# Performance work log

Hardware: AMD Instinct MI355X
Metric: run time of the kernel (lower is better)

Reference implementation:

```python
import jax, jax.numpy as jnp
import numpy as np

N, K, E, H, I = 4096, 2, 8, 2048, 1408  # tokens, top_k, experts, hidden, intermediate


def setup_inputs() -> dict:
    key = jax.random.key(0)
    kx, kl, kg, ku, kd = jax.random.split(key, 5)
    x = jax.random.normal(kx, (N, H), dtype=jnp.float32)
    # routing: distinct top-k expert ids per token (matches scatter_-based counting)
    logits = jax.random.normal(kl, (N, E), dtype=jnp.float32)
    top_vals, topk_ids = jax.lax.top_k(logits, K)
    topk_weight = jax.nn.softmax(top_vals, axis=-1)
    sH = 1.0 / np.sqrt(H).astype(np.float32)
    sI = 1.0 / np.sqrt(I).astype(np.float32)
    Wg = jax.random.normal(kg, (E, I, H), dtype=jnp.float32) * sH  # gate_proj per expert
    Wu = jax.random.normal(ku, (E, I, H), dtype=jnp.float32) * sH  # up_proj per expert
    Wd = jax.random.normal(kd, (E, H, I), dtype=jnp.float32) * sI  # down_proj per expert
    return {"x": x, "topk_ids": topk_ids.astype(jnp.int32), "topk_weight": topk_weight,
            "Wg": Wg, "Wu": Wu, "Wd": Wd}


def reference(x, topk_ids, topk_weight, Wg, Wu, Wd):
    # SwiGLU MLP for every expert on every token (dense reference for the
    # sort/dispatch/combine loop), then gather the top_k expert outputs and
    # combine with routing weights -- identical math to the torch module.
    g = jnp.einsum('nh,eih->eni', x, Wg)           # [E, N, I]
    u = jnp.einsum('nh,eih->eni', x, Wu)           # [E, N, I]
    hidden = jax.nn.silu(g) * u                    # fused SwiGLU
    out = jnp.einsum('eni,ehi->neh', hidden, Wd)   # [N, E, H]
    sel = jnp.take_along_axis(out, topk_ids[..., None].astype(jnp.int32), axis=1)  # [N, K, H]
    return jnp.sum(sel * topk_weight[..., None], axis=1)  # [N, H]
```

## Files before the change

### kernel.cpp

```cpp
#include <hip/hip_runtime.h>
#include <stdint.h>

#define N_TOK 4096
#define TOPK  2
#define NEXP  8
#define HID   2048
#define INTER 1408
#define NSLOT (N_TOK * TOPK)
#define PADROWS 128
#define WELEM (NEXP * INTER * HID)
#define MAXTILES 72

typedef _Float16 half8 __attribute__((ext_vector_type(8)));
typedef float floatx4 __attribute__((ext_vector_type(4)));

__device__ __forceinline__ void gld_lds16(const void* g, void* l) {
  __builtin_amdgcn_global_load_lds(
      (const __attribute__((address_space(1))) uint32_t*)g,
      (__attribute__((address_space(3))) uint32_t*)l, 16, 0, 0);
}

#define WAITCNT_VM6   0x0F76
#define WAITCNT_VM4   0x0F74
#define WAITCNT_VM0   0x0F70
#define WAITCNT_LGKM0 0xC07F
#define RAW_BARRIER() asm volatile("s_barrier" ::: "memory")

__global__ void route_kernel(const int* __restrict__ ids, const float* __restrict__ tw,
                             int* __restrict__ tinfo,
                             int* __restrict__ stok, float* __restrict__ sw) {
  __shared__ int tc[NEXP][257];
  __shared__ int eo[NEXP + 1];
  const int t = threadIdx.x;
  int lc[NEXP];
#pragma unroll
  for (int e = 0; e < NEXP; e++) lc[e] = 0;
  for (int i = 0; i < NSLOT / 256; i++) {
    int e = ids[t + 256 * i];
#pragma unroll
    for (int q = 0; q < NEXP; q++) lc[q] += (e == q) ? 1 : 0;
  }
#pragma unroll
  for (int e = 0; e < NEXP; e++) tc[e][t + 1] = lc[e];
  if (t < NEXP) tc[t][0] = 0;
  __syncthreads();
  if (t < NEXP) {
    int run = 0;
    for (int i = 0; i <= 256; i++) { run += tc[t][i]; tc[t][i] = run; }
  }
  __syncthreads();
  if (t == 0) {
    eo[0] = 0;
    for (int e = 0; e < NEXP; e++) eo[e + 1] = eo[e] + tc[e][256];
    int nt = 0;
    for (int e = 0; e < NEXP; e++) {
      const int c = tc[e][256];
      for (int r0 = 0; r0 < c; r0 += 128) {
        tinfo[1 + 3 * nt] = e;
        tinfo[2 + 3 * nt] = eo[e] + r0;
        tinfo[3 + 3 * nt] = (c - r0 < 128) ? (c - r0) : 128;
        nt++;
      }
    }
    tinfo[0] = nt;
  }
  __syncthreads();
  int pos[NEXP];
#pragma unroll
  for (int e = 0; e < NEXP; e++) pos[e] = eo[e] + tc[e][t];
  for (int i = 0; i < NSLOT / 256; i++) {
    int s = t + 256 * i;
    int e = ids[s];
    int p = 0;
#pragma unroll
    for (int q = 0; q < NEXP; q++)
      if (e == q) p = pos[q]++;
    stok[p] = s / TOPK;
    sw[p] = tw[s];
  }
}

__global__ void gather_x_kernel(const float* __restrict__ x, const int* __restrict__ stok,
                                _Float16* __restrict__ xg) {
  const int row = blockIdx.x;
  const int tok = stok[row];
  const float4* src = (const float4*)(x + (size_t)tok * HID);
  half8* dst = (half8*)(xg + (size_t)row * HID);
  const int t = threadIdx.x;
  float4 a = src[2 * t], b = src[2 * t + 1];
  half8 h;
  h[0] = (_Float16)a.x; h[1] = (_Float16)a.y; h[2] = (_Float16)a.z; h[3] = (_Float16)a.w;
  h[4] = (_Float16)b.x; h[5] = (_Float16)b.y; h[6] = (_Float16)b.z; h[7] = (_Float16)b.w;
  dst[t] = h;
}

__global__ void convert3_kernel(const float* __restrict__ s0, const float* __restrict__ s1,
                                const float* __restrict__ s2, _Float16* __restrict__ d0,
                                _Float16* __restrict__ d1, _Float16* __restrict__ d2) {
  const float* s = blockIdx.z == 0 ? s0 : (blockIdx.z == 1 ? s1 : s2);
  _Float16* d = blockIdx.z == 0 ? d0 : (blockIdx.z == 1 ? d1 : d2);
  const int j = (blockIdx.x * 256 + threadIdx.x) * 8;
  float4 a = *(const float4*)(s + j);
  float4 b = *(const float4*)(s + j + 4);
  half8 h;
  h[0] = (_Float16)a.x; h[1] = (_Float16)a.y; h[2] = (_Float16)a.z; h[3] = (_Float16)a.w;
  h[4] = (_Float16)b.x; h[5] = (_Float16)b.y; h[6] = (_Float16)b.z; h[7] = (_Float16)b.w;
  *(half8*)(d + j) = h;
}

__global__ void zero_kernel(float4* __restrict__ p, int n4) {
  int i = blockIdx.x * blockDim.x + threadIdx.x;
  int stride = gridDim.x * blockDim.x;
  for (; i < n4; i += stride) p[i] = make_float4(0.f, 0.f, 0.f, 0.f);
}

__global__ __launch_bounds__(256, 2) void gateup_kernel(
    const _Float16* __restrict__ A, const _Float16* __restrict__ Bg,
    const _Float16* __restrict__ Bu, _Float16* __restrict__ H,
    const int* __restrict__ tinfo) {
  const int nt = tinfo[0];
  const int ty = blockIdx.y;
  if (ty >= nt) return;
  const int e    = tinfo[1 + 3 * ty];
  const int row0 = tinfo[2 + 3 * ty];
  const int mrem = tinfo[3 + 3 * ty];
  const int col0 = blockIdx.x * 128;
  const _Float16* Bge = Bg + (size_t)e * INTER * HID;
  const _Float16* Bue = Bu + (size_t)e * INTER * HID;

  __shared__ __align__(16) _Float16 As[2][128 * 32];
  __shared__ __align__(16) _Float16 Bgs[2][128 * 32];
  __shared__ __align__(16) _Float16 Bus[2][128 * 32];

  const int tid = threadIdx.x;
  const int wave = tid >> 6, lane = tid & 63;
  const int quad = lane >> 4, l16 = lane & 15;
  const int wm = (wave >> 1) * 64, wn = (wave & 1) * 64;

  const int bo0 = wave * 2048 + lane * 16, bo1 = bo0 + 1024;
  const int ar0 = bo0 >> 6, ak0 = (bo0 & 63) >> 1;
  const int ar1 = bo1 >> 6, ak1 = (bo1 & 63) >> 1;
  const _Float16* Ab0 = A + (size_t)(row0 + ar0) * HID + ak0;
  const _Float16* Ab1 = A + (size_t)(row0 + ar1) * HID + ak1;
  const _Float16* Bg0 = Bge + (size_t)(col0 + ar0) * HID + ak0;
  const _Float16* Bg1 = Bge + (size_t)(col0 + ar1) * HID + ak1;
  const _Float16* Bu0 = Bue + (size_t)(col0 + ar0) * HID + ak0;
  const _Float16* Bu1 = Bue + (size_t)(col0 + ar1) * HID + ak1;

  floatx4 ag[4][4], au[4][4];
#pragma unroll
  for (int a = 0; a < 4; a++)
#pragma unroll
    for (int b = 0; b < 4; b++) {
      ag[a][b] = (floatx4){0.f, 0.f, 0.f, 0.f};
      au[a][b] = (floatx4){0.f, 0.f, 0.f, 0.f};
    }

  auto stage = [&](int kt, int buf) {
    const int k0 = kt * 32;
    char* as = (char*)(As[buf]) + wave * 2048;
    char* bg = (char*)(Bgs[buf]) + wave * 2048;
    char* bu = (char*)(Bus[buf]) + wave * 2048;
    gld_lds16(Ab0 + k0, as);
    gld_lds16(Ab1 + k0, as + 1024);
    gld_lds16(Bg0 + k0, bg);
    gld_lds16(Bg1 + k0, bg + 1024);
    gld_lds16(Bu0 + k0, bu);
    gld_lds16(Bu1 + k0, bu + 1024);
  };

  const int NKI = HID / 32;
  stage(0, 0);
  stage(1, 1);
  for (int kt = 0; kt < NKI; ++kt) {
    const int buf = kt & 1;
    if (kt < NKI - 1) __builtin_amdgcn_s_waitcnt(WAITCNT_VM6);
    else              __builtin_amdgcn_s_waitcnt(WAITCNT_VM0);
    RAW_BARRIER();
    half8 af[4], bgf[4], buf_[4];
#pragma unroll
    for (int i = 0; i < 4; ++i) {
      af[i]   = *(const half8*)(As[buf]  + (wm + i * 16 + l16) * 32 + quad * 8);
      bgf[i]  = *(const half8*)(Bgs[buf] + (wn + i * 16 + l16) * 32 + quad * 8);
      buf_[i] = *(const half8*)(Bus[buf] + (wn + i * 16 + l16) * 32 + quad * 8);
    }
    __builtin_amdgcn_s_waitcnt(WAITCNT_LGKM0);
    RAW_BARRIER();
    if (kt + 2 < NKI) stage(kt + 2, buf);
#pragma unroll
    for (int mi = 0; mi < 4; ++mi)
#pragma unroll
      for (int ni = 0; ni < 4; ++ni) {
        ag[mi][ni] = __builtin_amdgcn_mfma_f32_16x16x32_f16(af[mi], bgf[ni], ag[mi][ni], 0, 0, 0);
        au[mi][ni] = __builtin_amdgcn_mfma_f32_16x16x32_f16(af[mi], buf_[ni], au[mi][ni], 0, 0, 0);
      }
  }

#pragma unroll
  for (int mi = 0; mi < 4; ++mi)
#pragma unroll
    for (int r = 0; r < 4; ++r) {
      const int rm = wm + mi * 16 + quad * 4 + r;
      if (rm < mrem) {
        _Float16* hrow = H + (size_t)(row0 + rm) * INTER + col0 + wn;
#pragma unroll
        for (int ni = 0; ni < 4; ++ni) {
          float g = ag[mi][ni][r], u = au[mi][ni][r];
          float s = 1.0f / (1.0f + __expf(-g));
          hrow[ni * 16 + l16] = (_Float16)(g * s * u);
        }
      }
    }
}

__global__ __launch_bounds__(256, 3) void down_kernel(
    const _Float16* __restrict__ A, const _Float16* __restrict__ B, float* __restrict__ out,
    const int* __restrict__ tinfo, const int* __restrict__ stok, const float* __restrict__ sw) {
  const int nt = tinfo[0];
  const int ty = blockIdx.y;
  if (ty >= nt) return;
  const int e    = tinfo[1 + 3 * ty];
  const int row0 = tinfo[2 + 3 * ty];
  const int mrem = tinfo[3 + 3 * ty];
  const int col0 = blockIdx.x * 128;
  const _Float16* Be = B + (size_t)e * HID * INTER;

  __shared__ __align__(16) _Float16 As[2][128 * 32];
  __shared__ __align__(16) _Float16 Bs[2][128 * 32];

  const int tid = threadIdx.x;
  const int wave = tid >> 6, lane = tid & 63;
  const int quad = lane >> 4, l16 = lane & 15;
  const int wm = (wave >> 1) * 64, wn = (wave & 1) * 64;

  const int bo0 = wave * 2048 + lane * 16, bo1 = bo0 + 1024;
  const int ar0 = bo0 >> 6, ak0 = (bo0 & 63) >> 1;
  const int ar1 = bo1 >> 6, ak1 = (bo1 & 63) >> 1;
  const _Float16* Ab0 = A + (size_t)(row0 + ar0) * INTER + ak0;
  const _Float16* Ab1 = A + (size_t)(row0 + ar1) * INTER + ak1;
  const _Float16* Bb0 = Be + (size_t)(col0 + ar0) * INTER + ak0;
  const _Float16* Bb1 = Be + (size_t)(col0 + ar1) * INTER + ak1;

  floatx4 acc[4][4];
#pragma unroll
  for (int a = 0; a < 4; a++)
#pragma unroll
    for (int b = 0; b < 4; b++) acc[a][b] = (floatx4){0.f, 0.f, 0.f, 0.f};

  auto stage = [&](int kt, int buf) {
    const int k0 = kt * 32;
    char* as = (char*)(As[buf]) + wave * 2048;
    char* bs = (char*)(Bs[buf]) + wave * 2048;
    gld_lds16(Ab0 + k0, as);
    gld_lds16(Ab1 + k0, as + 1024);
    gld_lds16(Bb0 + k0, bs);
    gld_lds16(Bb1 + k0, bs + 1024);
  };

  const int NKI = INTER / 32;
  stage(0, 0);
  stage(1, 1);
  for (int kt = 0; kt < NKI; ++kt) {
    const int buf = kt & 1;
    if (kt < NKI - 1) __builtin_amdgcn_s_waitcnt(WAITCNT_VM4);
    else              __builtin_amdgcn_s_waitcnt(WAITCNT_VM0);
    RAW_BARRIER();
    half8 af[4], bf[4];
#pragma unroll
    for (int i = 0; i < 4; ++i) {
      af[i] = *(const half8*)(As[buf] + (wm + i * 16 + l16) * 32 + quad * 8);
      bf[i] = *(const half8*)(Bs[buf] + (wn + i * 16 + l16) * 32 + quad * 8);
    }
    __builtin_amdgcn_s_waitcnt(WAITCNT_LGKM0);
    RAW_BARRIER();
    if (kt + 2 < NKI) stage(kt + 2, buf);
#pragma unroll
    for (int mi = 0; mi < 4; ++mi)
#pragma unroll
      for (int ni = 0; ni < 4; ++ni)
        acc[mi][ni] = __builtin_amdgcn_mfma_f32_16x16x32_f16(af[mi], bf[ni], acc[mi][ni], 0, 0, 0);
  }

#pragma unroll
  for (int mi = 0; mi < 4; ++mi)
#pragma unroll
    for (int r = 0; r < 4; ++r) {
      const int rm = wm + mi * 16 + quad * 4 + r;
      if (rm < mrem) {
        const int slot = row0 + rm;
        const float wgt = sw[slot];
        float* orow = out + (size_t)stok[slot] * HID + col0 + wn;
#pragma unroll
        for (int ni = 0; ni < 4; ++ni) atomicAdd(&orow[ni * 16 + l16], wgt * acc[mi][ni][r]);
      }
    }
}

extern "C" void kernel_launch(void* const* d_in, const int* in_sizes, int n_in,
                              void* d_out, int out_size, void* d_ws, size_t ws_size,
                              hipStream_t stream) {
  const float* x   = (const float*)d_in[0];
  const int*   ids = (const int*)d_in[1];
  const float* tw  = (const float*)d_in[2];
  const float* Wg  = (const float*)d_in[3];
  const float* Wu  = (const float*)d_in[4];
  const float* Wd  = (const float*)d_in[5];
  float* out = (float*)d_out;

  char* ws = (char*)d_ws;
  size_t p = 0;
  auto alloc = [&](size_t bytes) -> void* {
    void* r = ws + p;
    p = (p + bytes + 255) & ~(size_t)255;
    return r;
  };
  int*   tinfo = (int*)alloc((1 + 3 * MAXTILES) * 4);
  int*   stok  = (int*)alloc(NSLOT * 4);
  float* sw    = (float*)alloc(NSLOT * 4);
  _Float16* Xg   = (_Float16*)alloc((size_t)(NSLOT + PADROWS) * HID * 2);
  _Float16* Hb   = (_Float16*)alloc((size_t)(NSLOT + PADROWS) * INTER * 2);
  _Float16* Wg16 = (_Float16*)alloc((size_t)WELEM * 2);
  _Float16* Wu16 = (_Float16*)alloc((size_t)WELEM * 2);
  _Float16* Wd16 = (_Float16*)alloc((size_t)WELEM * 2);
  (void)ws_size; (void)in_sizes; (void)n_in; (void)out_size;

  route_kernel<<<1, 256, 0, stream>>>(ids, tw, tinfo, stok, sw);
  gather_x_kernel<<<NSLOT, 256, 0, stream>>>(x, stok, Xg);
  convert3_kernel<<<dim3(WELEM / 8 / 256, 1, 3), 256, 0, stream>>>(Wg, Wu, Wd, Wg16, Wu16, Wd16);
  zero_kernel<<<2048, 256, 0, stream>>>((float4*)out, (N_TOK * HID) / 4);
  gateup_kernel<<<dim3(INTER / 128, MAXTILES), 256, 0, stream>>>(Xg, Wg16, Wu16, Hb, tinfo);
  down_kernel<<<dim3(HID / 128, MAXTILES), 256, 0, stream>>>(Hb, Wd16, out, tinfo, stok, sw);
}
```

Measured before the change: 628.8 us.

## Schedule GEMM tiles per XCD and replace atomic combine with gather kernel

The route kernel now builds a block schedule that assigns each (expert, column-strip) group of row tiles to one of 8 slots, balanced greedily by load. Block IDs are interleaved so that consecutive tiles of a strip land on the same XCD and share its L2, which is meant to improve weight reuse. The down GEMM stores fp16 per-slot results instead of doing float atomics, and a new combine kernel applies the routing weights per token. This removes the zero kernel and the atomic contention, at the cost of an extra fp16 intermediate buffer, an extra kernel launch and some precision loss from rounding to fp16 before the combine. Occupancy hints are also raised.

```diff
diff --git a/kernel.cpp b/kernel.cpp
--- a/kernel.cpp
+++ b/kernel.cpp
@@ -10,6 +10,12 @@
 #define PADROWS 128
 #define WELEM (NEXP * INTER * HID)
 #define MAXTILES 72
+#define NCOL_G (INTER / 128)
+#define NCOL_D (HID / 128)
+#define NSTRIP_G (NEXP * NCOL_G)
+#define NSTRIP_D (NEXP * NCOL_D)
+#define CAP 160
+#define GSCHED (8 * CAP)
 
 typedef _Float16 half8 __attribute__((ext_vector_type(8)));
 typedef float floatx4 __attribute__((ext_vector_type(4)));
@@ -27,10 +33,17 @@
 #define RAW_BARRIER() asm volatile("s_barrier" ::: "memory")
 
 __global__ void route_kernel(const int* __restrict__ ids, const float* __restrict__ tw,
-                             int* __restrict__ tinfo,
-                             int* __restrict__ stok, float* __restrict__ sw) {
+                             int* __restrict__ tinfo, int* __restrict__ stok,
+                             int* __restrict__ inv,
+                             int* __restrict__ schedG, int* __restrict__ schedD) {
   __shared__ int tc[NEXP][257];
   __shared__ int eo[NEXP + 1];
+  __shared__ int s_ft[NEXP], s_nt[NEXP];
+  __shared__ short g_x[NSTRIP_G], g_cx[NSTRIP_G];
+  __shared__ int   g_b[NSTRIP_G], g_ft[NSTRIP_G], g_n[NSTRIP_G];
+  __shared__ short d_x[NSTRIP_D], d_cx[NSTRIP_D];
+  __shared__ int   d_b[NSTRIP_D], d_ft[NSTRIP_D], d_n[NSTRIP_D];
+  __shared__ int nsg, nsd;
   const int t = threadIdx.x;
   int lc[NEXP];
 #pragma unroll
@@ -55,16 +68,52 @@
     int nt = 0;
     for (int e = 0; e < NEXP; e++) {
       const int c = tc[e][256];
+      s_ft[e] = nt;
       for (int r0 = 0; r0 < c; r0 += 128) {
         tinfo[1 + 3 * nt] = e;
         tinfo[2 + 3 * nt] = eo[e] + r0;
         tinfo[3 + 3 * nt] = (c - r0 < 128) ? (c - r0) : 128;
         nt++;
       }
+      s_nt[e] = nt - s_ft[e];
     }
     tinfo[0] = nt;
+    int loadg[8], loadd[8];
+    for (int x = 0; x < 8; x++) { loadg[x] = 0; loadd[x] = 0; }
+    int sg = 0, sd = 0;
+    for (int e = 0; e < NEXP; e++) {
+      const int n = s_nt[e];
+      if (n == 0) continue;
+      for (int cx = 0; cx < NCOL_G; cx++) {
+        int best = 0;
+        for (int x = 1; x < 8; x++) if (loadg[x] < loadg[best]) best = x;
+        g_x[sg] = (short)best; g_cx[sg] = (short)cx;
+        g_b[sg] = loadg[best]; g_ft[sg] = s_ft[e]; g_n[sg] = n;
+        loadg[best] += n; sg++;
+      }
+      for (int cx = 0; cx < NCOL_D; cx++) {
+        int best = 0;
+        for (int x = 1; x < 8; x++) if (loadd[x] < loadd[best]) best = x;
+        d_x[sd] = (short)best; d_cx[sd] = (short)cx;
+        d_b[sd] = loadd[best]; d_ft[sd] = s_ft[e]; d_n[sd] = n;
+        loadd[best] += n; sd++;
+      }
+    }
+    nsg = sg; nsd = sd;
   }
   __syncthreads();
+  for (int i = t; i < GSCHED; i += 256) { schedG[i] = -1; schedD[i] = -1; }
+  __syncthreads();
+  for (int s = 0; s < nsg; s++)
+    for (int i = t; i < g_n[s]; i += 256) {
+      int slot = g_b[s] + i;
+      if (slot < CAP) schedG[slot * 8 + g_x[s]] = ((int)g_cx[s] << 16) | (g_ft[s] + i);
+    }
+  for (int s = 0; s < nsd; s++)
+    for (int i = t; i < d_n[s]; i += 256) {
+      int slot = d_b[s] + i;
+      if (slot < CAP) schedD[slot * 8 + d_x[s]] = ((int)d_cx[s] << 16) | (d_ft[s] + i);
+    }
   int pos[NEXP];
 #pragma unroll
   for (int e = 0; e < NEXP; e++) pos[e] = eo[e] + tc[e][t];
@@ -76,7 +125,7 @@
     for (int q = 0; q < NEXP; q++)
       if (e == q) p = pos[q]++;
     stok[p] = s / TOPK;
-    sw[p] = tw[s];
+    inv[s] = p;
   }
 }
 
@@ -108,23 +157,17 @@
   *(half8*)(d + j) = h;
 }
 
-__global__ void zero_kernel(float4* __restrict__ p, int n4) {
-  int i = blockIdx.x * blockDim.x + threadIdx.x;
-  int stride = gridDim.x * blockDim.x;
-  for (; i < n4; i += stride) p[i] = make_float4(0.f, 0.f, 0.f, 0.f);
-}
-
-__global__ __launch_bounds__(256, 2) void gateup_kernel(
+__global__ __launch_bounds__(256, 3) void gateup_kernel(
     const _Float16* __restrict__ A, const _Float16* __restrict__ Bg,
     const _Float16* __restrict__ Bu, _Float16* __restrict__ H,
-    const int* __restrict__ tinfo) {
-  const int nt = tinfo[0];
-  const int ty = blockIdx.y;
-  if (ty >= nt) return;
-  const int e    = tinfo[1 + 3 * ty];
-  const int row0 = tinfo[2 + 3 * ty];
-  const int mrem = tinfo[3 + 3 * ty];
-  const int col0 = blockIdx.x * 128;
+    const int* __restrict__ tinfo, const int* __restrict__ sched) {
+  const int ent = sched[blockIdx.x];
+  if (ent < 0) return;
+  const int ti   = ent & 0xFFFF;
+  const int e    = tinfo[1 + 3 * ti];
+  const int row0 = tinfo[2 + 3 * ti];
+  const int mrem = tinfo[3 + 3 * ti];
+  const int col0 = (ent >> 16) * 128;
   const _Float16* Bge = Bg + (size_t)e * INTER * HID;
   const _Float16* Bue = Bu + (size_t)e * INTER * HID;
 
@@ -213,16 +256,17 @@
     }
 }
 
-__global__ __launch_bounds__(256, 3) void down_kernel(
-    const _Float16* __restrict__ A, const _Float16* __restrict__ B, float* __restrict__ out,
-    const int* __restrict__ tinfo, const int* __restrict__ stok, const float* __restrict__ sw) {
-  const int nt = tinfo[0];
-  const int ty = blockIdx.y;
-  if (ty >= nt) return;
-  const int e    = tinfo[1 + 3 * ty];
-  const int row0 = tinfo[2 + 3 * ty];
-  const int mrem = tinfo[3 + 3 * ty];
-  const int col0 = blockIdx.x * 128;
+__global__ __launch_bounds__(256, 4) void down_kernel(
+    const _Float16* __restrict__ A, const _Float16* __restrict__ B,
+    _Float16* __restrict__ Ds, const int* __restrict__ tinfo,
+    const int* __restrict__ sched) {
+  const int ent = sched[blockIdx.x];
+  if (ent < 0) return;
+  const int ti   = ent & 0xFFFF;
+  const int e    = tinfo[1 + 3 * ti];
+  const int row0 = tinfo[2 + 3 * ti];
+  const int mrem = tinfo[3 + 3 * ti];
+  const int col0 = (ent >> 16) * 128;
   const _Float16* Be = B + (size_t)e * HID * INTER;
 
   __shared__ __align__(16) _Float16 As[2][128 * 32];
@@ -287,13 +331,26 @@
     for (int r = 0; r < 4; ++r) {
       const int rm = wm + mi * 16 + quad * 4 + r;
       if (rm < mrem) {
-        const int slot = row0 + rm;
-        const float wgt = sw[slot];
-        float* orow = out + (size_t)stok[slot] * HID + col0 + wn;
-#pragma unroll
-        for (int ni = 0; ni < 4; ++ni) atomicAdd(&orow[ni * 16 + l16], wgt * acc[mi][ni][r]);
-      }
-    }
+        _Float16* drow = Ds + (size_t)(row0 + rm) * HID + col0 + wn;
+#pragma unroll
+        for (int ni = 0; ni < 4; ++ni) drow[ni * 16 + l16] = (_Float16)acc[mi][ni][r];
+      }
+    }
+}
+
+__global__ void combine_kernel(const _Float16* __restrict__ Ds, const int* __restrict__ inv,
+                               const float* __restrict__ tw, float* __restrict__ out) {
+  const int tok = blockIdx.x, t = threadIdx.x;
+  const int p0 = inv[2 * tok], p1 = inv[2 * tok + 1];
+  const float w0 = tw[2 * tok], w1 = tw[2 * tok + 1];
+  half8 a = ((const half8*)(Ds + (size_t)p0 * HID))[t];
+  half8 b = ((const half8*)(Ds + (size_t)p1 * HID))[t];
+  float o[8];
+#pragma unroll
+  for (int i = 0; i < 8; i++) o[i] = w0 * (float)a[i] + w1 * (float)b[i];
+  float* orow = out + (size_t)tok * HID + t * 8;
+  *(float4*)orow = make_float4(o[0], o[1], o[2], o[3]);
+  *(float4*)(orow + 4) = make_float4(o[4], o[5], o[6], o[7]);
 }
 
 extern "C" void kernel_launch(void* const* d_in, const int* in_sizes, int n_in,
@@ -314,20 +371,23 @@
     p = (p + bytes + 255) & ~(size_t)255;
     return r;
   };
-  int*   tinfo = (int*)alloc((1 + 3 * MAXTILES) * 4);
-  int*   stok  = (int*)alloc(NSLOT * 4);
-  float* sw    = (float*)alloc(NSLOT * 4);
+  int*   tinfo  = (int*)alloc((1 + 3 * MAXTILES) * 4);
+  int*   stok   = (int*)alloc(NSLOT * 4);
+  int*   inv    = (int*)alloc(NSLOT * 4);
+  int*   schedG = (int*)alloc(GSCHED * 4);
+  int*   schedD = (int*)alloc(GSCHED * 4);
   _Float16* Xg   = (_Float16*)alloc((size_t)(NSLOT + PADROWS) * HID * 2);
   _Float16* Hb   = (_Float16*)alloc((size_t)(NSLOT + PADROWS) * INTER * 2);
+  _Float16* Dsb  = (_Float16*)alloc((size_t)(NSLOT + PADROWS) * HID * 2);
   _Float16* Wg16 = (_Float16*)alloc((size_t)WELEM * 2);
   _Float16* Wu16 = (_Float16*)alloc((size_t)WELEM * 2);
   _Float16* Wd16 = (_Float16*)alloc((size_t)WELEM * 2);
   (void)ws_size; (void)in_sizes; (void)n_in; (void)out_size;
 
-  route_kernel<<<1, 256, 0, stream>>>(ids, tw, tinfo, stok, sw);
+  route_kernel<<<1, 256, 0, stream>>>(ids, tw, tinfo, stok, inv, schedG, schedD);
   gather_x_kernel<<<NSLOT, 256, 0, stream>>>(x, stok, Xg);
   convert3_kernel<<<dim3(WELEM / 8 / 256, 1, 3), 256, 0, stream>>>(Wg, Wu, Wd, Wg16, Wu16, Wd16);
-  zero_kernel<<<2048, 256, 0, stream>>>((float4*)out, (N_TOK * HID) / 4);
-  gateup_kernel<<<dim3(INTER / 128, MAXTILES), 256, 0, stream>>>(Xg, Wg16, Wu16, Hb, tinfo);
-  down_kernel<<<dim3(HID / 128, MAXTILES), 256, 0, stream>>>(Hb, Wd16, out, tinfo, stok, sw);
-}
+  gateup_kernel<<<GSCHED, 256, 0, stream>>>(Xg, Wg16, Wu16, Hb, tinfo, schedG);
+  down_kernel<<<GSCHED, 256, 0, stream>>>(Hb, Wd16, Dsb, tinfo, schedD);
+  combine_kernel<<<N_TOK, 256, 0, stream>>>(Dsb, inv, tw, out);
+}
```

Measured after the change: 724.7 us. 1.15x slower.
